# Performance work log

Measured on AMD Instinct MI355X. Metric: run time of the kernel, lower is better.

Reference implementation:

```python
import jax, jax.numpy as jnp
import numpy as np

DIM, H, K, RADIUS = 128, 4, 32, 0.3
DH = DIM // H
N, M = 16384, 4096


def setup_inputs() -> dict:
    key = jax.random.key(0)
    ks = jax.random.split(key, 16)
    s = 0.02
    return {
        "xyz": jax.random.normal(ks[0], (N, 3), jnp.float32),
        "feats": jax.random.normal(ks[1], (N, DIM), jnp.float32),
        "idx_center": jax.random.randint(ks[2], (M,), 0, N, jnp.int64),
        "Wq": jax.random.normal(ks[3], (DIM, DIM), jnp.float32) * s,
        "Wk": jax.random.normal(ks[4], (DIM, DIM), jnp.float32) * s,
        "Wv": jax.random.normal(ks[5], (DIM, DIM), jnp.float32) * s,
        "Wo": jax.random.normal(ks[6], (DIM, DIM), jnp.float32) * s,
        "bo": jnp.zeros((DIM,), jnp.float32),
        "g1": jnp.ones((DIM,), jnp.float32),
        "be1": jnp.zeros((DIM,), jnp.float32),
        "g2": jnp.ones((DIM,), jnp.float32),
        "be2": jnp.zeros((DIM,), jnp.float32),
        "W1": jax.random.normal(ks[7], (4 * DIM, DIM), jnp.float32) * s,
        "b1f": jnp.zeros((4 * DIM,), jnp.float32),
        "W2": jax.random.normal(ks[8], (DIM, 4 * DIM), jnp.float32) * s,
        "b2f": jnp.zeros((DIM,), jnp.float32),
    }


def _layernorm(x, g, b, eps=1e-5):
    mu = x.mean(-1, keepdims=True)
    var = ((x - mu) ** 2).mean(-1, keepdims=True)
    return (x - mu) / jnp.sqrt(var + eps) * g + b


def reference(xyz, feats, idx_center, Wq, Wk, Wv, Wo, bo, g1, be1, g2, be2, W1, b1f, W2, b2f):
    m = idx_center.shape[0]
    c_xyz = xyz[idx_center]          # (M,3)
    c_feat = feats[idx_center]       # (M,DIM)
    # pairwise Euclidean distance (M,N), like torch.cdist
    d2 = (jnp.sum(c_xyz * c_xyz, -1)[:, None] + jnp.sum(xyz * xyz, -1)[None, :]
          - 2.0 * (c_xyz @ xyz.T))
    dist = jnp.sqrt(jnp.maximum(d2, 1e-12))
    mask = dist < RADIUS
    mask = mask.at[jnp.arange(m), idx_center].set(True)  # force self-inclusion
    dmask = jnp.where(mask, dist, jnp.inf)
    neg_d, nbr_idx = jax.lax.top_k(-dmask, K)            # k smallest distances
    nbr_dist = -neg_d
    valid = jnp.isfinite(nbr_dist)                       # (M,K)
    nbr_feats = jnp.where(valid[..., None], feats[nbr_idx], 0.0)  # (M,K,DIM)
    # tiny per-center attention
    q = (c_feat @ Wq.T).reshape(m, H, DH)
    k = (nbr_feats @ Wk.T).reshape(m, K, H, DH).transpose(0, 2, 1, 3)  # (M,H,K,DH)
    v = (nbr_feats @ Wv.T).reshape(m, K, H, DH).transpose(0, 2, 1, 3)
    attn = jnp.einsum('mhd,mhkd->mhk', q * (DH ** -0.5), k)
    attn = jnp.where(valid[:, None, :], attn, -1e9)
    attn = jax.nn.softmax(attn, axis=-1)
    out = jnp.einsum('mhk,mhkd->mhd', attn, v)
    out = out.transpose(0, 2, 1).reshape(m, DIM)  # matches torch transpose(1,2).reshape
    upd = out @ Wo.T + bo
    c_feat = c_feat + _layernorm(upd, g1, be1)
    ffn = jax.nn.relu(c_feat @ W1.T + b1f) @ W2.T + b2f
    c_feat = c_feat + _layernorm(ffn, g2, be2)
    nearest = jnp.argmin(dist, axis=0)            # (N,) nearest center per point
    return feats + c_feat[nearest]
```

## Files before the change

### kernel.cpp

```cpp
#include <hip/hip_runtime.h>
#include <hip/hip_bf16.h>

#define DIMF 128
#define KNBR 32
#define NH 4
#define DH 32
#define RADIUS 0.3f
#define CB 8
#define CAND 256
#define PPB 32

#define PACK_BLOCKS 140

typedef unsigned long long u64t;

__device__ __forceinline__ void tr4_tile(const float4* __restrict__ in4, float4* __restrict__ out4,
                                         int AI, int BI, int a0, int b0, int t, char* smem) {
    float4(*tile)[33] = (float4(*)[33])smem;
    int tx = t & 31, ty = t >> 5;
    for (int r = ty; r < 32; r += 8) tile[r][tx] = in4[(long)(b0 + r) * AI + a0 + tx];
    __syncthreads();
    for (int r = ty; r < 32; r += 8) out4[(long)(a0 + r) * BI + b0 + tx] = tile[tx][r];
}

__global__ __launch_bounds__(256) void pack_kernel(
    const float* __restrict__ xyz, const int* __restrict__ idxc,
    const float* __restrict__ Wq, const float* __restrict__ Wv,
    const float* __restrict__ Wo, const float* __restrict__ W1,
    const float* __restrict__ W2, const float* __restrict__ Wk,
    float4* __restrict__ qp4, float4* __restrict__ vp4, float4* __restrict__ op4,
    float4* __restrict__ w1p4, float4* __restrict__ w2p4, float4* __restrict__ kp4,
    float4* __restrict__ xyz4, float4* __restrict__ cds4, int N, int M) {
    __shared__ __align__(16) char smem[16896];
    int pk = blockIdx.x, t = threadIdx.x;
    if (pk < 4) {
        tr4_tile((const float4*)Wq, qp4, 32, 128, 0, pk * 32, t, smem);
    } else if (pk < 8) {
        tr4_tile((const float4*)Wv, vp4, 32, 128, 0, (pk - 4) * 32, t, smem);
    } else if (pk < 12) {
        tr4_tile((const float4*)Wo, op4, 32, 128, 0, (pk - 8) * 32, t, smem);
    } else if (pk < 28) {
        tr4_tile((const float4*)W1, w1p4, 32, 512, 0, (pk - 12) * 32, t, smem);
    } else if (pk < 44) {
        int i = pk - 28;
        tr4_tile((const float4*)W2, w2p4, 128, 128, (i >> 2) * 32, (i & 3) * 32, t, smem);
    } else if (pk < 60) {
        int idx = (pk - 44) * 256 + t;
        int q = idx >> 7, j = idx & 127;
        float4 w;
        w.x = Wk[(long)(4 * q + 0) * DIMF + j];
        w.y = Wk[(long)(4 * q + 1) * DIMF + j];
        w.z = Wk[(long)(4 * q + 2) * DIMF + j];
        w.w = Wk[(long)(4 * q + 3) * DIMF + j];
        kp4[q * DIMF + j] = w;
    } else if (pk < 124) {
        int idx = (pk - 60) * 256 + t;
        if (idx < N) {
            float x = xyz[3 * idx], y = xyz[3 * idx + 1], z = xyz[3 * idx + 2];
            xyz4[idx] = make_float4(x, y, z, (x * x + y * y) + z * z);
        }
    } else {
        int idx = (pk - 124) * 256 + t;
        if (idx < M) {
            int ic = idxc[idx];
            float cx = xyz[3 * ic], cy = xyz[3 * ic + 1], cz = xyz[3 * ic + 2];
            cds4[idx] = make_float4(-2.0f * cx, -2.0f * cy, -2.0f * cz,
                                    (cx * cx + cy * cy) + cz * cz);
        }
    }
}

__global__ __launch_bounds__(256) void main_kernel(
    const float4* __restrict__ xyz4, const float4* __restrict__ cds4g,
    const float* __restrict__ feats, const int* __restrict__ idxc,
    const float4* __restrict__ qp4, const float4* __restrict__ kp4,
    const float4* __restrict__ vp4, const float4* __restrict__ op4,
    const float* __restrict__ bo, const float* __restrict__ g1,
    const float* __restrict__ be1, const float* __restrict__ g2,
    const float* __restrict__ be2, const float4* __restrict__ w1p4,
    const float* __restrict__ b1f, const float4* __restrict__ w2p4,
    const float* __restrict__ b2f, float* __restrict__ cfin,
    int* __restrict__ bestm, int N, int M) {
    __shared__ __align__(16) char smem[32768];
    __shared__ int nbrl[CB][KNBR];
    __shared__ int cnt[CB];

    int t = threadIdx.x;
    int b = blockIdx.x;
    int nAttn = M / CB;

    if (b >= nAttn) {
        float4* cds = (float4*)smem;
        int pt = t >> 3, q = t & 7;
        int n = (b - nAttn) * PPB + pt;
        float4 p4 = xyz4[n];
        float px = p4.x, py = p4.y, pz = p4.z;
        float bd0 = INFINITY, bd1 = INFINITY;
        int bm0 = 0, bm1 = 0;
        for (int c0 = 0; c0 < M; c0 += 1024) {
            __syncthreads();
            for (int i = t; i < 1024; i += 256) cds[i] = cds4g[c0 + i];
            __syncthreads();
#pragma unroll 8
            for (int i = 0; i < 64; ++i) {
                int ci0 = q + (2 * i) * 8, ci1 = q + (2 * i + 1) * 8;
                float4 ca = cds[ci0];
                float4 cb = cds[ci1];
                float sa = fmaf(ca.x, px, fmaf(ca.y, py, fmaf(ca.z, pz, ca.w)));
                float sb = fmaf(cb.x, px, fmaf(cb.y, py, fmaf(cb.z, pz, cb.w)));
                if (sa < bd0) { bd0 = sa; bm0 = c0 + ci0; }
                if (sb < bd1) { bd1 = sb; bm1 = c0 + ci1; }
            }
        }
        if (bd1 < bd0 || (bd1 == bd0 && bm1 < bm0)) { bd0 = bd1; bm0 = bm1; }
#pragma unroll
        for (int o = 1; o < 8; o <<= 1) {
            float obd = __shfl_xor(bd0, o);
            int obm = __shfl_xor(bm0, o);
            if (obd < bd0 || (obd == bd0 && obm < bm0)) { bd0 = obd; bm0 = obm; }
        }
        if (q == 0) bestm[n] = bm0;
        return;
    }

    int m0 = b * CB;

    {
        u64t(*cand)[CAND] = (u64t(*)[CAND])smem;
        if (t < CB) cnt[t] = 0;
        __syncthreads();
        float nx[CB], ny[CB], nz[CB], cw[CB];
#pragma unroll
        for (int tc = 0; tc < CB; ++tc) {
            float4 c4v = cds4g[m0 + tc];
            nx[tc] = c4v.x; ny[tc] = c4v.y; nz[tc] = c4v.z; cw[tc] = c4v.w;
        }
        const float R2 = RADIUS * RADIUS;
        for (int n = t; n < N; n += 256) {
            float4 p4 = xyz4[n];
            float rhs = R2 - p4.w;
#pragma unroll
            for (int tc = 0; tc < CB; ++tc) {
                float s = fmaf(nx[tc], p4.x, fmaf(ny[tc], p4.y, fmaf(nz[tc], p4.z, cw[tc])));
                if (s < rhs) {
                    int pos = atomicAdd(&cnt[tc], 1);
                    if (pos < CAND)
                        cand[tc][pos] = (((u64t)__float_as_uint(fmaxf(s + p4.w, 0.0f))) << 32) | (unsigned)n;
                }
            }
        }
        __syncthreads();
        int w = t >> 6, lane = t & 63;
        for (int rep = 0; rep < 2; ++rep) {
            int cidx = w + rep * 4;
            int C = cnt[cidx] < CAND ? cnt[cidx] : CAND;
            const u64t* vc = cand[cidx];
            if (C <= 64) {
                u64t mykey = (lane < C) ? vc[lane] : ~0ull;
                int rank = 0;
                for (int j = 0; j < C; ++j) rank += (vc[j] < mykey) ? 1 : 0;
                if (lane < C && rank < KNBR) nbrl[cidx][rank] = (int)(mykey & 0xffffffffu);
                if (lane >= C && lane < KNBR) nbrl[cidx][lane] = -1;
            } else {
                u64t mykey[4];
                int myrank[4];
#pragma unroll
                for (int s = 0; s < 4; ++s) {
                    int i = s * 64 + lane;
                    mykey[s] = (i < C) ? vc[i] : ~0ull;
                    myrank[s] = 0;
                }
                for (int j = 0; j < C; ++j) {
                    u64t kj = vc[j];
#pragma unroll
                    for (int s = 0; s < 4; ++s) myrank[s] += (kj < mykey[s]) ? 1 : 0;
                }
#pragma unroll
                for (int s = 0; s < 4; ++s) {
                    int i = s * 64 + lane;
                    if (i < C && myrank[s] < KNBR) nbrl[cidx][myrank[s]] = (int)(mykey[s] & 0xffffffffu);
                }
            }
        }
    }
    __syncthreads();

    float(*cf)[DIMF] = (float(*)[DIMF])smem;
    float(*cf2)[DIMF] = (float(*)[DIMF])(smem + 4096);
    float(*S1)[4 * DIMF] = (float(*)[4 * DIMF])(smem + 8192);
    float(*S2)[DIMF] = (float(*)[DIMF])(smem + 24576);
    float(*S3)[DIMF] = (float(*)[DIMF])(smem + 28672);

    int lane127 = t & 127;
    int cg = (t >> 7) * 4;
    int c8 = t >> 5, k32 = t & 31;

    {
        int ic = idxc[m0 + c8];
        *(float4*)&cf[c8][k32 * 4] = *(const float4*)&feats[(long)ic * DIMF + k32 * 4];
    }
    __syncthreads();

    {
        float acc[4] = {0.f, 0.f, 0.f, 0.f};
        for (int jj = 0; jj < 32; ++jj) {
            float4 w = qp4[jj * DIMF + lane127];
#pragma unroll
            for (int cc = 0; cc < 4; ++cc) {
                float4 x = *(const float4*)&cf[cg + cc][jj * 4];
                acc[cc] += w.x * x.x + w.y * x.y + w.z * x.z + w.w * x.w;
            }
        }
#pragma unroll
        for (int cc = 0; cc < 4; ++cc) S2[cg + cc][lane127] = acc[cc] * 0.17677669529663687f;
    }
    __syncthreads();

    {
        int j = lane127, hs = t >> 7;
#pragma unroll
        for (int hh = 0; hh < 2; ++hh) {
            int h = hs * 2 + hh;
            float acc[8] = {0.f, 0.f, 0.f, 0.f, 0.f, 0.f, 0.f, 0.f};
            for (int d4 = 0; d4 < 8; ++d4) {
                float4 w = kp4[(h * 8 + d4) * DIMF + j];
#pragma unroll
                for (int c = 0; c < 8; ++c) {
                    float4 qv = *(const float4*)&S2[c][h * DH + d4 * 4];
                    acc[c] += qv.x * w.x + qv.y * w.y + qv.z * w.z + qv.w * w.w;
                }
            }
#pragma unroll
            for (int c = 0; c < 8; ++c) S1[c][h * DIMF + j] = acc[c];
        }
    }
    __syncthreads();

    {
        int ni = nbrl[c8][k32];
        const float* nrow = feats + (long)(ni < 0 ? 0 : ni) * DIMF;
        float lg[4] = {0.f, 0.f, 0.f, 0.f};
        for (int jj = 0; jj < 32; ++jj) {
            float4 f = *(const float4*)&nrow[jj * 4];
#pragma unroll
            for (int h = 0; h < 4; ++h) {
                float4 qwv = *(const float4*)&S1[c8][h * DIMF + jj * 4];
                lg[h] += f.x * qwv.x + f.y * qwv.y + f.z * qwv.z + f.w * qwv.w;
            }
        }
        if (ni < 0) { lg[0] = -1e9f; lg[1] = -1e9f; lg[2] = -1e9f; lg[3] = -1e9f; }
#pragma unroll
        for (int h = 0; h < 4; ++h) {
            float mx = lg[h];
            for (int o = 16; o; o >>= 1) mx = fmaxf(mx, __shfl_xor(mx, o, 32));
            float e = expf(lg[h] - mx);
            float s = e;
            for (int o = 16; o; o >>= 1) s += __shfl_xor(s, o, 32);
            S3[c8][h * KNBR + k32] = e / s;
        }
    }
    __syncthreads();

    {
        int j4 = k32 * 4;
        float a0x = 0.f, a0y = 0.f, a0z = 0.f, a0w = 0.f;
        float a1x = 0.f, a1y = 0.f, a1z = 0.f, a1w = 0.f;
        float a2x = 0.f, a2y = 0.f, a2z = 0.f, a2w = 0.f;
        float a3x = 0.f, a3y = 0.f, a3z = 0.f, a3w = 0.f;
        for (int k = 0; k < KNBR; ++k) {
            int ni = nbrl[c8][k];
            const float* nrow = feats + (long)(ni < 0 ? 0 : ni) * DIMF;
            float4 f = *(const float4*)&nrow[j4];
            float w0 = S3[c8][0 * KNBR + k], w1 = S3[c8][1 * KNBR + k];
            float w2 = S3[c8][2 * KNBR + k], w3 = S3[c8][3 * KNBR + k];
            a0x += w0 * f.x; a0y += w0 * f.y; a0z += w0 * f.z; a0w += w0 * f.w;
            a1x += w1 * f.x; a1y += w1 * f.y; a1z += w1 * f.z; a1w += w1 * f.w;
            a2x += w2 * f.x; a2y += w2 * f.y; a2z += w2 * f.z; a2w += w2 * f.w;
            a3x += w3 * f.x; a3y += w3 * f.y; a3z += w3 * f.z; a3w += w3 * f.w;
        }
        __syncthreads();
        *(float4*)&S1[c8][0 * DIMF + j4] = make_float4(a0x, a0y, a0z, a0w);
        *(float4*)&S1[c8][1 * DIMF + j4] = make_float4(a1x, a1y, a1z, a1w);
        *(float4*)&S1[c8][2 * DIMF + j4] = make_float4(a2x, a2y, a2z, a2w);
        *(float4*)&S1[c8][3 * DIMF + j4] = make_float4(a3x, a3y, a3z, a3w);
    }
    __syncthreads();

    {
        int i = lane127, h = i >> 5, d = i & 31;
        float acc[4] = {0.f, 0.f, 0.f, 0.f};
        for (int jj = 0; jj < 32; ++jj) {
            float4 w = vp4[jj * DIMF + i];
#pragma unroll
            for (int cc = 0; cc < 4; ++cc) {
                float4 pv = *(const float4*)&S1[cg + cc][h * DIMF + jj * 4];
                acc[cc] += w.x * pv.x + w.y * pv.y + w.z * pv.z + w.w * pv.w;
            }
        }
        __syncthreads();
#pragma unroll
        for (int cc = 0; cc < 4; ++cc) S2[cg + cc][d * NH + h] = acc[cc];
    }
    __syncthreads();

    {
        int i = lane127;
        float acc[4] = {0.f, 0.f, 0.f, 0.f};
        for (int jj = 0; jj < 32; ++jj) {
            float4 w = op4[jj * DIMF + i];
#pragma unroll
            for (int cc = 0; cc < 4; ++cc) {
                float4 x = *(const float4*)&S2[cg + cc][jj * 4];
                acc[cc] += w.x * x.x + w.y * x.y + w.z * x.z + w.w * x.w;
            }
        }
        float b = bo[i];
        __syncthreads();
#pragma unroll
        for (int cc = 0; cc < 4; ++cc) S3[cg + cc][i] = acc[cc] + b;
    }
    __syncthreads();

    {
        int i4 = k32 * 4;
        float4 u = *(const float4*)&S3[c8][i4];
        float s = ((u.x + u.y) + u.z) + u.w;
        for (int o = 16; o; o >>= 1) s += __shfl_xor(s, o, 32);
        float mu = s * (1.0f / DIMF);
        float d0 = u.x - mu, d1 = u.y - mu, d2 = u.z - mu, d3 = u.w - mu;
        float vs = ((d0 * d0 + d1 * d1) + d2 * d2) + d3 * d3;
        for (int o = 16; o; o >>= 1) vs += __shfl_xor(vs, o, 32);
        float rs = 1.0f / sqrtf(vs * (1.0f / DIMF) + 1e-5f);
        float4 g = *(const float4*)&g1[i4];
        float4 b = *(const float4*)&be1[i4];
        float4 base = *(const float4*)&cf[c8][i4];
        float4 r;
        r.x = base.x + d0 * rs * g.x + b.x;
        r.y = base.y + d1 * rs * g.y + b.y;
        r.z = base.z + d2 * rs * g.z + b.z;
        r.w = base.w + d3 * rs * g.w + b.w;
        *(float4*)&cf2[c8][i4] = r;
    }
    __syncthreads();

    {
        int u0 = lane127;
        float acc[4][4];
#pragma unroll
        for (int p = 0; p < 4; ++p)
#pragma unroll
            for (int cc = 0; cc < 4; ++cc) acc[p][cc] = 0.f;
        for (int jj = 0; jj < 32; ++jj) {
            float4 x[4];
#pragma unroll
            for (int cc = 0; cc < 4; ++cc) x[cc] = *(const float4*)&cf2[cg + cc][jj * 4];
#pragma unroll
            for (int p = 0; p < 4; ++p) {
                float4 w = w1p4[jj * 512 + u0 + p * DIMF];
#pragma unroll
                for (int cc = 0; cc < 4; ++cc)
                    acc[p][cc] += w.x * x[cc].x + w.y * x[cc].y + w.z * x[cc].z + w.w * x[cc].w;
            }
        }
#pragma unroll
        for (int p = 0; p < 4; ++p) {
            float b = b1f[u0 + p * DIMF];
#pragma unroll
            for (int cc = 0; cc < 4; ++cc)
                S1[cg + cc][u0 + p * DIMF] = fmaxf(acc[p][cc] + b, 0.f);
        }
    }
    __syncthreads();

    {
        int i = lane127;
        float acc[4] = {0.f, 0.f, 0.f, 0.f};
        for (int uu = 0; uu < 128; ++uu) {
            float4 w = w2p4[uu * DIMF + i];
#pragma unroll
            for (int cc = 0; cc < 4; ++cc) {
                float4 hh = *(const float4*)&S1[cg + cc][uu * 4];
                acc[cc] += w.x * hh.x + w.y * hh.y + w.z * hh.z + w.w * hh.w;
            }
        }
        float b = b2f[i];
        __syncthreads();
#pragma unroll
        for (int cc = 0; cc < 4; ++cc) S3[cg + cc][i] = acc[cc] + b;
    }
    __syncthreads();

    {
        int i4 = k32 * 4;
        float4 u = *(const float4*)&S3[c8][i4];
        float s = ((u.x + u.y) + u.z) + u.w;
        for (int o = 16; o; o >>= 1) s += __shfl_xor(s, o, 32);
        float mu = s * (1.0f / DIMF);
        float d0 = u.x - mu, d1 = u.y - mu, d2 = u.z - mu, d3 = u.w - mu;
        float vs = ((d0 * d0 + d1 * d1) + d2 * d2) + d3 * d3;
        for (int o = 16; o; o >>= 1) vs += __shfl_xor(vs, o, 32);
        float rs = 1.0f / sqrtf(vs * (1.0f / DIMF) + 1e-5f);
        float4 g = *(const float4*)&g2[i4];
        float4 b = *(const float4*)&be2[i4];
        float4 base = *(const float4*)&cf2[c8][i4];
        float4 r;
        r.x = base.x + d0 * rs * g.x + b.x;
        r.y = base.y + d1 * rs * g.y + b.y;
        r.z = base.z + d2 * rs * g.z + b.z;
        r.w = base.w + d3 * rs * g.w + b.w;
        *(float4*)&cfin[(long)(m0 + c8) * DIMF + i4] = r;
    }
}

__global__ __launch_bounds__(256) void out_kernel(const float4* __restrict__ feats4,
                                                  const float* __restrict__ cfin,
                                                  const int* __restrict__ bestm,
                                                  float4* __restrict__ out4, int total) {
    int idx = blockIdx.x * 256 + threadIdx.x;
    if (idx >= total) return;
    int n = idx >> 5, c = idx & 31;
    const float4* cf4 = (const float4*)cfin;
    float4 f = feats4[idx];
    float4 g = cf4[(long)bestm[n] * 32 + c];
    out4[idx] = make_float4(f.x + g.x, f.y + g.y, f.z + g.z, f.w + g.w);
}

extern "C" void kernel_launch(void* const* d_in, const int* in_sizes, int n_in,
                              void* d_out, int out_size, void* d_ws, size_t ws_size,
                              hipStream_t stream) {
    const float* xyz = (const float*)d_in[0];
    const float* feats = (const float*)d_in[1];
    const int* idxc = (const int*)d_in[2];
    const float* Wq = (const float*)d_in[3];
    const float* Wk = (const float*)d_in[4];
    const float* Wv = (const float*)d_in[5];
    const float* Wo = (const float*)d_in[6];
    const float* bo = (const float*)d_in[7];
    const float* g1 = (const float*)d_in[8];
    const float* be1 = (const float*)d_in[9];
    const float* g2 = (const float*)d_in[10];
    const float* be2 = (const float*)d_in[11];
    const float* W1 = (const float*)d_in[12];
    const float* b1f = (const float*)d_in[13];
    const float* W2 = (const float*)d_in[14];
    const float* b2f = (const float*)d_in[15];

    int N = in_sizes[0] / 3;
    int M = in_sizes[2];

    char* ws = (char*)d_ws;
    size_t off = 0;
    float* cfin = (float*)(ws + off); off += (size_t)M * DIMF * 4;
    int* bestm = (int*)(ws + off); off += (size_t)N * 4;
    float4* qp4 = (float4*)(ws + off); off += (size_t)DIMF * DIMF * 4;
    float4* vp4 = (float4*)(ws + off); off += (size_t)DIMF * DIMF * 4;
    float4* op4 = (float4*)(ws + off); off += (size_t)DIMF * DIMF * 4;
    float4* kp4 = (float4*)(ws + off); off += (size_t)DIMF * DIMF * 4;
    float4* w1p4 = (float4*)(ws + off); off += (size_t)4 * DIMF * DIMF * 4;
    float4* w2p4 = (float4*)(ws + off); off += (size_t)4 * DIMF * DIMF * 4;
    float4* xyz4 = (float4*)(ws + off); off += (size_t)N * 16;
    float4* cds4 = (float4*)(ws + off); off += (size_t)M * 16;
    (void)ws_size; (void)n_in; (void)out_size;

    pack_kernel<<<PACK_BLOCKS, 256, 0, stream>>>(
        xyz, idxc, Wq, Wv, Wo, W1, W2, Wk,
        qp4, vp4, op4, w1p4, w2p4, kp4, xyz4, cds4, N, M);
    main_kernel<<<M / CB + N / PPB, 256, 0, stream>>>(
        xyz4, cds4, feats, idxc, qp4, kp4, vp4, op4, bo, g1, be1, g2, be2,
        w1p4, b1f, w2p4, b2f, cfin, bestm, N, M);
    out_kernel<<<(N * DIMF / 4 + 255) / 256, 256, 0, stream>>>(
        (const float4*)feats, cfin, bestm, (float4*)d_out, N * DIMF / 4);
}
```

Measured before the change: 190.2 us.

## Run FFN matmuls on fp16 MFMA with prepacked half-precision weights

The per-block FFN (W1 and W2 GEMMs over 8 centers) moves from scalar fp32 FMA loops to 16x16x32 fp16 MFMA instructions. The pack kernel now converts W1 and W2 to fp16 fragments in MFMA lane order, and the normalized activations and hidden layer are staged in swizzled fp16 shared memory. This cuts ALU work and halves weight traffic, but lowers precision to fp16 inputs and pads the 8-center tile to 16 MFMA rows.

```diff
diff --git a/kernel.cpp b/kernel.cpp
--- a/kernel.cpp
+++ b/kernel.cpp
@@ -10,9 +10,12 @@
 #define CAND 256
 #define PPB 32
 
-#define PACK_BLOCKS 140
+#define PACK_BLOCKS 172
 
 typedef unsigned long long u64t;
+typedef _Float16 f16x8 __attribute__((ext_vector_type(8)));
+typedef _Float16 f16x4 __attribute__((ext_vector_type(4)));
+typedef float f32x4 __attribute__((ext_vector_type(4)));
 
 __device__ __forceinline__ void tr4_tile(const float4* __restrict__ in4, float4* __restrict__ out4,
                                          int AI, int BI, int a0, int b0, int t, char* smem) {
@@ -29,7 +32,7 @@
     const float* __restrict__ Wo, const float* __restrict__ W1,
     const float* __restrict__ W2, const float* __restrict__ Wk,
     float4* __restrict__ qp4, float4* __restrict__ vp4, float4* __restrict__ op4,
-    float4* __restrict__ w1p4, float4* __restrict__ w2p4, float4* __restrict__ kp4,
+    float4* __restrict__ kp4, f16x8* __restrict__ w1h, f16x8* __restrict__ w2h,
     float4* __restrict__ xyz4, float4* __restrict__ cds4, int N, int M) {
     __shared__ __align__(16) char smem[16896];
     int pk = blockIdx.x, t = threadIdx.x;
@@ -40,12 +43,7 @@
     } else if (pk < 12) {
         tr4_tile((const float4*)Wo, op4, 32, 128, 0, (pk - 8) * 32, t, smem);
     } else if (pk < 28) {
-        tr4_tile((const float4*)W1, w1p4, 32, 512, 0, (pk - 12) * 32, t, smem);
-    } else if (pk < 44) {
-        int i = pk - 28;
-        tr4_tile((const float4*)W2, w2p4, 128, 128, (i >> 2) * 32, (i & 3) * 32, t, smem);
-    } else if (pk < 60) {
-        int idx = (pk - 44) * 256 + t;
+        int idx = (pk - 12) * 256 + t;
         int q = idx >> 7, j = idx & 127;
         float4 w;
         w.x = Wk[(long)(4 * q + 0) * DIMF + j];
@@ -53,20 +51,40 @@
         w.z = Wk[(long)(4 * q + 2) * DIMF + j];
         w.w = Wk[(long)(4 * q + 3) * DIMF + j];
         kp4[q * DIMF + j] = w;
-    } else if (pk < 124) {
-        int idx = (pk - 60) * 256 + t;
+    } else if (pk < 92) {
+        int idx = (pk - 28) * 256 + t;
         if (idx < N) {
             float x = xyz[3 * idx], y = xyz[3 * idx + 1], z = xyz[3 * idx + 2];
             xyz4[idx] = make_float4(x, y, z, (x * x + y * y) + z * z);
         }
-    } else {
-        int idx = (pk - 124) * 256 + t;
+    } else if (pk < 108) {
+        int idx = (pk - 92) * 256 + t;
         if (idx < M) {
             int ic = idxc[idx];
             float cx = xyz[3 * ic], cy = xyz[3 * ic + 1], cz = xyz[3 * ic + 2];
             cds4[idx] = make_float4(-2.0f * cx, -2.0f * cy, -2.0f * cz,
                                     (cx * cx + cy * cy) + cz * cz);
         }
+    } else if (pk < 140) {
+        int e = (pk - 108) * 256 + t;
+        int l = e & 63, ks = (e >> 6) & 3, nt = e >> 8;
+        int row = nt * 16 + (l & 15);
+        int cb = ks * 32 + (l >> 4) * 8;
+        const float* src = W1 + (long)row * DIMF + cb;
+        f16x8 v;
+#pragma unroll
+        for (int j = 0; j < 8; ++j) v[j] = (_Float16)src[j];
+        w1h[e] = v;
+    } else {
+        int e = (pk - 140) * 256 + t;
+        int l = e & 63, ks = (e >> 6) & 15, nt = e >> 10;
+        int row = nt * 16 + (l & 15);
+        int cb = ks * 32 + (l >> 4) * 8;
+        const float* src = W2 + (long)row * (4 * DIMF) + cb;
+        f16x8 v;
+#pragma unroll
+        for (int j = 0; j < 8; ++j) v[j] = (_Float16)src[j];
+        w2h[e] = v;
     }
 }
 
@@ -77,8 +95,8 @@
     const float4* __restrict__ vp4, const float4* __restrict__ op4,
     const float* __restrict__ bo, const float* __restrict__ g1,
     const float* __restrict__ be1, const float* __restrict__ g2,
-    const float* __restrict__ be2, const float4* __restrict__ w1p4,
-    const float* __restrict__ b1f, const float4* __restrict__ w2p4,
+    const float* __restrict__ be2, const f16x8* __restrict__ w1h,
+    const float* __restrict__ b1f, const f16x8* __restrict__ w2h,
     const float* __restrict__ b2f, float* __restrict__ cfin,
     int* __restrict__ bestm, int N, int M) {
     __shared__ __align__(16) char smem[32768];
@@ -340,53 +358,69 @@
         r.z = base.z + d2 * rs * g.z + b.z;
         r.w = base.w + d3 * rs * g.w + b.w;
         *(float4*)&cf2[c8][i4] = r;
-    }
-    __syncthreads();
-
-    {
-        int u0 = lane127;
-        float acc[4][4];
-#pragma unroll
-        for (int p = 0; p < 4; ++p)
-#pragma unroll
-            for (int cc = 0; cc < 4; ++cc) acc[p][cc] = 0.f;
-        for (int jj = 0; jj < 32; ++jj) {
-            float4 x[4];
-#pragma unroll
-            for (int cc = 0; cc < 4; ++cc) x[cc] = *(const float4*)&cf2[cg + cc][jj * 4];
-#pragma unroll
-            for (int p = 0; p < 4; ++p) {
-                float4 w = w1p4[jj * 512 + u0 + p * DIMF];
-#pragma unroll
-                for (int cc = 0; cc < 4; ++cc)
-                    acc[p][cc] += w.x * x[cc].x + w.y * x[cc].y + w.z * x[cc].z + w.w * x[cc].w;
-            }
-        }
-#pragma unroll
-        for (int p = 0; p < 4; ++p) {
-            float b = b1f[u0 + p * DIMF];
-#pragma unroll
-            for (int cc = 0; cc < 4; ++cc)
-                S1[cg + cc][u0 + p * DIMF] = fmaxf(acc[p][cc] + b, 0.f);
-        }
-    }
-    __syncthreads();
-
-    {
-        int i = lane127;
-        float acc[4] = {0.f, 0.f, 0.f, 0.f};
-        for (int uu = 0; uu < 128; ++uu) {
-            float4 w = w2p4[uu * DIMF + i];
-#pragma unroll
-            for (int cc = 0; cc < 4; ++cc) {
-                float4 hh = *(const float4*)&S1[cg + cc][uu * 4];
-                acc[cc] += w.x * hh.x + w.y * hh.y + w.z * hh.z + w.w * hh.w;
-            }
-        }
-        float b = b2f[i];
-        __syncthreads();
-#pragma unroll
-        for (int cc = 0; cc < 4; ++cc) S3[cg + cc][i] = acc[cc] + b;
+        {
+            int byteoff = (c8 * 256 + i4 * 2) ^ ((c8 & 7) << 4);
+            f16x4 hv = {(_Float16)r.x, (_Float16)r.y, (_Float16)r.z, (_Float16)r.w};
+            *(f16x4*)(smem + 24576 + byteoff) = hv;
+        }
+    }
+    __syncthreads();
+
+    {
+        int lane = t & 63, w = t >> 6;
+        int la = lane & 15, kg = lane >> 4;
+        f16x8 afr[4];
+#pragma unroll
+        for (int ks = 0; ks < 4; ++ks) {
+            int byteoff = (la * 256 + ks * 64 + kg * 16) ^ ((la & 7) << 4);
+            afr[ks] = *(const f16x8*)(smem + 24576 + byteoff);
+        }
+#pragma unroll
+        for (int nt0 = 0; nt0 < 8; ++nt0) {
+            int nt = w * 8 + nt0;
+            f32x4 acc = {0.f, 0.f, 0.f, 0.f};
+#pragma unroll
+            for (int ks = 0; ks < 4; ++ks) {
+                f16x8 bfr = w1h[(nt * 4 + ks) * 64 + lane];
+                acc = __builtin_amdgcn_mfma_f32_16x16x32_f16(afr[ks], bfr, acc, 0, 0, 0);
+            }
+            int col = nt * 16 + la;
+            float bb = b1f[col];
+#pragma unroll
+            for (int r = 0; r < 4; ++r) {
+                int row = kg * 4 + r;
+                float v = fmaxf(acc[r] + bb, 0.f);
+                int byteoff = (row * 1024 + col * 2) ^ ((row & 7) << 4);
+                *(_Float16*)(smem + 8192 + byteoff) = (_Float16)v;
+            }
+        }
+    }
+    __syncthreads();
+
+    {
+        int lane = t & 63, w = t >> 6;
+        int la = lane & 15, kg = lane >> 4;
+        int nt0 = w * 2, nt1 = w * 2 + 1;
+        f32x4 acc0 = {0.f, 0.f, 0.f, 0.f}, acc1 = {0.f, 0.f, 0.f, 0.f};
+#pragma unroll
+        for (int ks = 0; ks < 16; ++ks) {
+            int byteoff = (la * 1024 + ks * 64 + kg * 16) ^ ((la & 7) << 4);
+            f16x8 afr = *(const f16x8*)(smem + 8192 + byteoff);
+            f16x8 b0 = w2h[(nt0 * 16 + ks) * 64 + lane];
+            f16x8 b1v = w2h[(nt1 * 16 + ks) * 64 + lane];
+            acc0 = __builtin_amdgcn_mfma_f32_16x16x32_f16(afr, b0, acc0, 0, 0, 0);
+            acc1 = __builtin_amdgcn_mfma_f32_16x16x32_f16(afr, b1v, acc1, 0, 0, 0);
+        }
+        if (lane < 32) {
+            float bb0 = b2f[nt0 * 16 + la];
+            float bb1 = b2f[nt1 * 16 + la];
+#pragma unroll
+            for (int r = 0; r < 4; ++r) {
+                int row = kg * 4 + r;
+                S3[row][nt0 * 16 + la] = acc0[r] + bb0;
+                S3[row][nt1 * 16 + la] = acc1[r] + bb1;
+            }
+        }
     }
     __syncthreads();
 
@@ -456,18 +490,18 @@
     float4* vp4 = (float4*)(ws + off); off += (size_t)DIMF * DIMF * 4;
     float4* op4 = (float4*)(ws + off); off += (size_t)DIMF * DIMF * 4;
     float4* kp4 = (float4*)(ws + off); off += (size_t)DIMF * DIMF * 4;
-    float4* w1p4 = (float4*)(ws + off); off += (size_t)4 * DIMF * DIMF * 4;
-    float4* w2p4 = (float4*)(ws + off); off += (size_t)4 * DIMF * DIMF * 4;
+    f16x8* w1h = (f16x8*)(ws + off); off += (size_t)8192 * 16;
+    f16x8* w2h = (f16x8*)(ws + off); off += (size_t)8192 * 16;
     float4* xyz4 = (float4*)(ws + off); off += (size_t)N * 16;
     float4* cds4 = (float4*)(ws + off); off += (size_t)M * 16;
     (void)ws_size; (void)n_in; (void)out_size;
 
     pack_kernel<<<PACK_BLOCKS, 256, 0, stream>>>(
         xyz, idxc, Wq, Wv, Wo, W1, W2, Wk,
-        qp4, vp4, op4, w1p4, w2p4, kp4, xyz4, cds4, N, M);
+        qp4, vp4, op4, kp4, w1h, w2h, xyz4, cds4, N, M);
     main_kernel<<<M / CB + N / PPB, 256, 0, stream>>>(
         xyz4, cds4, feats, idxc, qp4, kp4, vp4, op4, bo, g1, be1, g2, be2,
-        w1p4, b1f, w2p4, b2f, cfin, bestm, N, M);
+        w1h, b1f, w2h, b2f, cfin, bestm, N, M);
     out_kernel<<<(N * DIMF / 4 + 255) / 256, 256, 0, stream>>>(
         (const float4*)feats, cfin, bestm, (float4*)d_out, N * DIMF / 4);
 }
```

After: 167.9 us. -11.7%, faster.
